# Performance work log

Hardware: AMD Instinct MI355X
Metric: run time of the kernel (lower is better)

The kernel has to match this reference:

```python
import jax, jax.numpy as jnp
import numpy as np

NEG_SLOPE = 0.2
LN_EPS = 1e-5


def setup_inputs() -> dict:
    key = jax.random.key(0)
    k1, k2, k3, k4 = jax.random.split(key, 4)
    B, K, D, H = 64, 256, 1024, 2
    x = jax.random.normal(k1, (B, K, D), dtype=jnp.float32)
    adj = jax.random.randint(k2, (K, K), 0, 2, dtype=jnp.int32)
    # Xavier-ish scaling for weights
    W = jax.random.normal(k3, (D, D), dtype=jnp.float32) * (1.0 / np.sqrt(D))
    a = jax.random.normal(k4, (H, 2 * D), dtype=jnp.float32) * (1.0 / np.sqrt(2 * D))
    gamma = jnp.ones((D,), dtype=jnp.float32)
    beta = jnp.zeros((D,), dtype=jnp.float32)
    return {"x": x, "adj": adj, "W": W, "a": a, "gamma": gamma, "beta": beta}


def _layer_norm(y, gamma, beta):
    mu = jnp.mean(y, axis=-1, keepdims=True)
    var = jnp.mean(jnp.square(y - mu), axis=-1, keepdims=True)
    return (y - mu) * jax.lax.rsqrt(var + LN_EPS) * gamma + beta


def reference(x, adj, W, a, gamma, beta):
    # x: (B,K,D), adj: (K,K), W: (D,D), a: (H,2D)
    D = W.shape[1]
    h = jnp.einsum("bki,io->bko", x, W)  # (B,K,D)
    # GAT trick: a^T [h_i; h_j] = a_src . h_i + a_dst . h_j (same math as
    # the huge pairwise-concat + Linear in the original module).
    a_src, a_dst = a[:, :D], a[:, D:]  # each (H,D)
    f_i = jnp.einsum("bkd,hd->bhk", h, a_src)  # (B,H,K)
    f_j = jnp.einsum("bkd,hd->bhk", h, a_dst)  # (B,H,K)
    e = f_i[:, :, :, None] + f_j[:, :, None, :]  # (B,H,K,K)
    e = jnp.where(e >= 0, e, NEG_SLOPE * e)  # LeakyReLU
    mask = (adj != 0)[None, None]  # (1,1,K,K)
    e = jnp.where(mask, e, -jnp.inf)
    attn = jax.nn.softmax(e, axis=-1)
    attn = jnp.where(jnp.isnan(attn), 0.0, attn)  # nan_to_num for all-masked rows
    # dropout is identity in eval mode
    head_out = jnp.einsum("bhij,bjd->bhid", attn, h)  # (B,H,K,D)
    out = jnp.mean(head_out, axis=1)  # average heads, (B,K,D)
    out = _layer_norm(out + x, gamma, beta)  # residual is Identity (in_dim==out_dim)
    return out
```

## Files before the change

### kernel.cpp

```cpp
#include <hip/hip_runtime.h>
#include <hip/hip_bf16.h>

#define KN 256
#define DD 1024
#define HH 2

typedef __attribute__((ext_vector_type(8))) short short8;
typedef __attribute__((ext_vector_type(4))) float f32x4;

__device__ __forceinline__ ushort f2b(float f) {
  union { float f; unsigned u; } v; v.f = f;
  unsigned u = v.u;
  return (ushort)((u + 0x7fffu + ((u >> 16) & 1u)) >> 16);
}
__device__ __forceinline__ float b2f(ushort h) {
  union { unsigned u; float f; } v; v.u = ((unsigned)h) << 16;
  return v.f;
}
__device__ __forceinline__ void gload16(const ushort* g, ushort* l) {
  __builtin_amdgcn_global_load_lds(
      (const __attribute__((address_space(1))) void*)g,
      (__attribute__((address_space(3))) void*)l, 16, 0, 0);
}

__global__ __launch_bounds__(256) void k_conv(const float* __restrict__ x,
                                              ushort* __restrict__ xb) {
  int c0 = blockIdx.x * 256 + threadIdx.x;
  for (int it = 0; it < 4; ++it) {
    size_t i = ((size_t)c0 + (size_t)it * 524288) * 8;
    float4 v0 = *reinterpret_cast<const float4*>(&x[i]);
    float4 v1 = *reinterpret_cast<const float4*>(&x[i + 4]);
    short8 o;
    o[0] = (short)f2b(v0.x); o[1] = (short)f2b(v0.y);
    o[2] = (short)f2b(v0.z); o[3] = (short)f2b(v0.w);
    o[4] = (short)f2b(v1.x); o[5] = (short)f2b(v1.y);
    o[6] = (short)f2b(v1.z); o[7] = (short)f2b(v1.w);
    *reinterpret_cast<short8*>(&xb[i]) = o;
  }
}

__global__ __launch_bounds__(256) void k_wT(const float* __restrict__ W, ushort* __restrict__ WTb) {
  __shared__ float t[32][33];
  int tx = threadIdx.x, ty = threadIdx.y;
  int x = blockIdx.x * 32 + tx;
  int y0 = blockIdx.y * 32 + ty;
  for (int i = 0; i < 32; i += 8)
    t[ty + i][tx] = W[(size_t)(y0 + i) * DD + x];
  __syncthreads();
  int xo = blockIdx.y * 32 + tx;
  int yo = blockIdx.x * 32 + ty;
  for (int i = 0; i < 32; i += 8)
    WTb[(size_t)(yo + i) * DD + xo] = f2b(t[tx][ty + i]);
}

__device__ __forceinline__ void gh_stage(const ushort* gA0, const ushort* gB0, int kt,
                                         ushort* As, ushort* Bs, int tid) {
  int wb = tid & ~63;
  for (int it = 0; it < 2; ++it) {
    int slot = it * 256 + tid;
    int row = slot >> 2, kc = slot & 3;
    int kcs = kc ^ (((row >> 1) & 1) << 1);
    gload16(gA0 + (size_t)row * DD + kt + kcs * 8, As + (size_t)(it * 256 + wb) * 8);
    gload16(gB0 + (size_t)row * DD + kt + kcs * 8, Bs + (size_t)(it * 256 + wb) * 8);
  }
}

__global__ __launch_bounds__(256) void k_gemm_h(const ushort* __restrict__ xb,
                                                const ushort* __restrict__ WTb,
                                                ushort* __restrict__ hT) {
  __shared__ ushort As[2][4096];
  __shared__ ushort Bs[2][4096];
  const int tid = threadIdx.x;
  const int bm = blockIdx.x;
  const int bn = blockIdx.y;
  const int w = tid >> 6, lane = tid & 63;
  const int wm = (w >> 1) * 64, wn = (w & 1) * 64;
  const int r16 = lane & 15, kqi = lane >> 4;
  const ushort* gA0 = xb + (size_t)(bm * 128) * DD;
  const ushort* gB0 = WTb + (size_t)(bn * 128) * DD;
  f32x4 acc[4][4] = {};

  gh_stage(gA0, gB0, 0, As[0], Bs[0], tid);
  __syncthreads();
  for (int kt = 0; kt < DD; kt += 32) {
    int cur = (kt >> 5) & 1;
    if (kt + 32 < DD)
      gh_stage(gA0, gB0, kt + 32, As[cur ^ 1], Bs[cur ^ 1], tid);
    const ushort* Ac = As[cur];
    const ushort* Bc = Bs[cur];
    short8 af[4], bf[4];
    for (int mf = 0; mf < 4; ++mf) {
      int row = wm + mf * 16 + r16;
      af[mf] = *reinterpret_cast<const short8*>(Ac + row * 32 + (kqi ^ (((row >> 1) & 1) << 1)) * 8);
    }
    for (int nf = 0; nf < 4; ++nf) {
      int row = wn + nf * 16 + r16;
      bf[nf] = *reinterpret_cast<const short8*>(Bc + row * 32 + (kqi ^ (((row >> 1) & 1) << 1)) * 8);
    }
    for (int mf = 0; mf < 4; ++mf)
      for (int nf = 0; nf < 4; ++nf)
        acc[mf][nf] = __builtin_amdgcn_mfma_f32_16x16x32_bf16(af[mf], bf[nf], acc[mf][nf], 0, 0, 0);
    __syncthreads();
  }
  const int b = bm >> 1;
  const int j0base = (bm & 1) * 128 + wm;
  for (int mf = 0; mf < 4; ++mf) {
    int j0 = j0base + mf * 16 + (lane >> 4) * 4;
    for (int nf = 0; nf < 4; ++nf) {
      int C = bn * 128 + wn + nf * 16 + r16;
      ushort4 o;
      o.x = f2b(acc[mf][nf][0]); o.y = f2b(acc[mf][nf][1]);
      o.z = f2b(acc[mf][nf][2]); o.w = f2b(acc[mf][nf][3]);
      *reinterpret_cast<ushort4*>(&hT[((size_t)b * DD + C) * KN + j0]) = o;
    }
  }
}

__global__ __launch_bounds__(256) void k_f(const ushort* __restrict__ hT,
                                           const float* __restrict__ a,
                                           float* __restrict__ fip, float* __restrict__ fjp) {
  __shared__ float als[4][256];
  int b = blockIdx.x, dq = blockIdx.y;
  int tid = threadIdx.x;
  for (int v = 0; v < 4; ++v) als[v][tid] = a[v * DD + dq * 256 + tid];
  __syncthreads();
  const ushort* base = hT + ((size_t)b * DD + dq * 256) * KN + tid;
  float a0 = 0.f, a1 = 0.f, a2 = 0.f, a3 = 0.f;
  #pragma unroll 8
  for (int d = 0; d < 256; ++d) {
    float hv = b2f(base[(size_t)d * KN]);
    a0 += hv * als[0][d];
    a1 += hv * als[1][d];
    a2 += hv * als[2][d];
    a3 += hv * als[3][d];
  }
  size_t o = ((size_t)(dq * 64 + b) * HH) * KN + tid;
  fip[o] = a0;
  fjp[o] = a1;
  fip[o + KN] = a2;
  fjp[o + KN] = a3;
}

__global__ __launch_bounds__(256) void k_attn(const float* __restrict__ fip, const float* __restrict__ fjp,
                                              const int* __restrict__ adj, ushort* __restrict__ Pb) {
  int w = threadIdx.x >> 6, l = threadIdx.x & 63;
  int gw = blockIdx.x * 4 + w;
  int b = gw >> 8, i = gw & 255;
  int4 am = *reinterpret_cast<const int4*>(adj + i * KN + l * 4);
  int msk[4] = { am.x, am.y, am.z, am.w };
  float fi0 = 0.f, fi1 = 0.f;
  float fj0[4] = {0.f, 0.f, 0.f, 0.f}, fj1[4] = {0.f, 0.f, 0.f, 0.f};
  for (int dq = 0; dq < 4; ++dq) {
    size_t o = ((size_t)(dq * 64 + b) * HH) * KN;
    fi0 += fip[o + i];
    fi1 += fip[o + KN + i];
    float4 t0 = *reinterpret_cast<const float4*>(&fjp[o + l * 4]);
    float4 t1 = *reinterpret_cast<const float4*>(&fjp[o + KN + l * 4]);
    fj0[0] += t0.x; fj0[1] += t0.y; fj0[2] += t0.z; fj0[3] += t0.w;
    fj1[0] += t1.x; fj1[1] += t1.y; fj1[2] += t1.z; fj1[3] += t1.w;
  }
  float e0[4], e1[4];
  const float NEGINF = -3.0e38f;
  float m0 = NEGINF, m1 = NEGINF;
  for (int e = 0; e < 4; ++e) {
    float v0 = fi0 + fj0[e], v1 = fi1 + fj1[e];
    v0 = v0 >= 0.f ? v0 : 0.2f * v0;
    v1 = v1 >= 0.f ? v1 : 0.2f * v1;
    e0[e] = v0; e1[e] = v1;
    if (msk[e]) { m0 = fmaxf(m0, v0); m1 = fmaxf(m1, v1); }
  }
  for (int off = 1; off < 64; off <<= 1) {
    m0 = fmaxf(m0, __shfl_xor(m0, off));
    m1 = fmaxf(m1, __shfl_xor(m1, off));
  }
  float p0[4], p1[4], s0 = 0.f, s1 = 0.f;
  for (int e = 0; e < 4; ++e) {
    p0[e] = msk[e] ? __expf(e0[e] - m0) : 0.f;
    p1[e] = msk[e] ? __expf(e1[e] - m1) : 0.f;
    s0 += p0[e]; s1 += p1[e];
  }
  for (int off = 1; off < 64; off <<= 1) {
    s0 += __shfl_xor(s0, off);
    s1 += __shfl_xor(s1, off);
  }
  float i0 = s0 > 0.f ? 1.f / s0 : 0.f;
  float i1 = s1 > 0.f ? 1.f / s1 : 0.f;
  ushort4 o;
  o.x = f2b(0.5f * (p0[0] * i0 + p1[0] * i1));
  o.y = f2b(0.5f * (p0[1] * i0 + p1[1] * i1));
  o.z = f2b(0.5f * (p0[2] * i0 + p1[2] * i1));
  o.w = f2b(0.5f * (p0[3] * i0 + p1[3] * i1));
  *reinterpret_cast<ushort4*>(&Pb[((size_t)b * KN + i) * KN + l * 4]) = o;
}

__global__ __launch_bounds__(512) void k_gemm_o(const ushort* __restrict__ Pb,
                                                const ushort* __restrict__ hT,
                                                const float* __restrict__ x,
                                                ushort* __restrict__ y,
                                                float* __restrict__ pstats) {
  __shared__ ushort As[2][8192];
  __shared__ ushort Bs[2][4096];
  __shared__ float red2[256][2][2];
  const int b = blockIdx.x;
  const int dt = blockIdx.y;
  const int tid = threadIdx.x;
  const int w = tid >> 6, lane = tid & 63;
  const int wm = (w >> 1) * 64;
  const int wn = (w & 1) * 64;
  const int r16 = lane & 15, kqi = lane >> 4;
  const ushort* PbB = Pb + (size_t)b * KN * KN;
  const ushort* hTB = hT + ((size_t)b * DD + dt * 128) * KN;
  f32x4 acc[4][4] = {};

  const int wb = tid & ~63;
  #define OSTAGE(buf, kt)                                                          \
    {                                                                              \
      for (int it = 0; it < 2; ++it) {                                             \
        int slot = it * 512 + tid;                                                 \
        int row = slot >> 2, kc = slot & 3;                                        \
        int kcs = kc ^ (((row >> 1) & 1) << 1);                                    \
        gload16(PbB + (size_t)row * KN + (kt) + kcs * 8,                           \
                As[buf] + (size_t)(it * 512 + wb) * 8);                            \
      }                                                                            \
      {                                                                            \
        int row = tid >> 2, kc = tid & 3;                                          \
        int kcs = kc ^ (((row >> 1) & 1) << 1);                                    \
        gload16(hTB + (size_t)row * KN + (kt) + kcs * 8,                           \
                Bs[buf] + (size_t)wb * 8);                                         \
      }                                                                            \
    }

  OSTAGE(0, 0);
  __syncthreads();
  for (int kt = 0; kt < KN; kt += 32) {
    int cur = (kt >> 5) & 1;
    if (kt + 32 < KN)
      OSTAGE(cur ^ 1, kt + 32);
    const ushort* Ac = As[cur];
    const ushort* Bc = Bs[cur];
    short8 af[4], bf[4];
    for (int mf = 0; mf < 4; ++mf) {
      int row = wm + mf * 16 + r16;
      af[mf] = *reinterpret_cast<const short8*>(Ac + (size_t)row * 32 + (kqi ^ (((row >> 1) & 1) << 1)) * 8);
    }
    for (int nf = 0; nf < 4; ++nf) {
      int row = wn + nf * 16 + r16;
      bf[nf] = *reinterpret_cast<const short8*>(Bc + (size_t)row * 32 + (kqi ^ (((row >> 1) & 1) << 1)) * 8);
    }
    for (int mf = 0; mf < 4; ++mf)
      for (int nf = 0; nf < 4; ++nf)
        acc[mf][nf] = __builtin_amdgcn_mfma_f32_16x16x32_bf16(af[mf], bf[nf], acc[mf][nf], 0, 0, 0);
    __syncthreads();
  }
  #undef OSTAGE

  const int g = lane >> 4;
  float ps[4][4] = {}, qs[4][4] = {};
  #pragma unroll
  for (int mf = 0; mf < 4; ++mf)
    #pragma unroll
    for (int nf = 0; nf < 4; ++nf) {
      int C = dt * 128 + wn + nf * 16 + r16;
      #pragma unroll
      for (int rr = 0; rr < 4; ++rr) {
        int i = wm + mf * 16 + g * 4 + rr;
        size_t gi = ((size_t)(b * KN + i)) * DD + C;
        float v = acc[mf][nf][rr] + x[gi];
        y[gi] = f2b(v);
        ps[mf][rr] += v; qs[mf][rr] += v * v;
      }
    }
  #pragma unroll
  for (int off = 1; off < 16; off <<= 1)
    #pragma unroll
    for (int mf = 0; mf < 4; ++mf)
      #pragma unroll
      for (int rr = 0; rr < 4; ++rr) {
        ps[mf][rr] += __shfl_xor(ps[mf][rr], off);
        qs[mf][rr] += __shfl_xor(qs[mf][rr], off);
      }
  if (r16 == 0) {
    #pragma unroll
    for (int mf = 0; mf < 4; ++mf)
      #pragma unroll
      for (int rr = 0; rr < 4; ++rr) {
        int i = wm + mf * 16 + g * 4 + rr;
        red2[i][w & 1][0] = ps[mf][rr];
        red2[i][w & 1][1] = qs[mf][rr];
      }
  }
  __syncthreads();
  if (tid < 256) {
    float S = red2[tid][0][0] + red2[tid][1][0];
    float Q = red2[tid][0][1] + red2[tid][1][1];
    size_t o = ((size_t)(dt * 64 + b) * KN + tid) * 2;
    pstats[o] = S;
    pstats[o + 1] = Q;
  }
}

__global__ __launch_bounds__(256) void k_ln(const ushort* __restrict__ y,
                                            const float* __restrict__ pstats,
                                            const float* __restrict__ gamma,
                                            const float* __restrict__ beta,
                                            float* __restrict__ out) {
  int tid = threadIdx.x;
  size_t row = blockIdx.x;
  int b = (int)(row >> 8), i = (int)(row & 255);
  float S = 0.f, Q = 0.f;
  #pragma unroll
  for (int dt = 0; dt < 8; ++dt) {
    size_t o = ((size_t)(dt * 64 + b) * KN + i) * 2;
    S += pstats[o];
    Q += pstats[o + 1];
  }
  float mu = S * (1.0f / DD);
  float var = Q * (1.0f / DD) - mu * mu;
  float inv = rsqrtf(var + 1e-5f);
  ushort4 v = *reinterpret_cast<const ushort4*>(&y[row * DD + tid * 4]);
  float4 gm = *reinterpret_cast<const float4*>(&gamma[tid * 4]);
  float4 bt = *reinterpret_cast<const float4*>(&beta[tid * 4]);
  float4 o;
  o.x = (b2f(v.x) - mu) * inv * gm.x + bt.x;
  o.y = (b2f(v.y) - mu) * inv * gm.y + bt.y;
  o.z = (b2f(v.z) - mu) * inv * gm.z + bt.z;
  o.w = (b2f(v.w) - mu) * inv * gm.w + bt.w;
  *reinterpret_cast<float4*>(&out[row * DD + tid * 4]) = o;
}

extern "C" void kernel_launch(void* const* d_in, const int* in_sizes, int n_in,
                              void* d_out, int out_size, void* d_ws, size_t ws_size,
                              hipStream_t stream) {
  const float* x     = (const float*)d_in[0];
  const int*   adj   = (const int*)d_in[1];
  const float* W     = (const float*)d_in[2];
  const float* a     = (const float*)d_in[3];
  const float* gamma = (const float*)d_in[4];
  const float* beta  = (const float*)d_in[5];
  float* out = (float*)d_out;

  char* ws = (char*)d_ws;
  const size_t OFS_WT = 0;
  const size_t OFS_XB = 2097152;
  const size_t OFS_HT = 35651584;
  const size_t OFS_PB = 69206016;
  const size_t NEED   = 77856768;
  if (ws_size < NEED) return;

  ushort* WTb   = (ushort*)(ws + OFS_WT);
  float*  fip   = (float*)(ws + OFS_WT);
  float*  fjp   = (float*)(ws + OFS_WT + 524288);
  float*  pst   = (float*)(ws + OFS_WT);
  ushort* xb    = (ushort*)(ws + OFS_XB);
  ushort* y     = (ushort*)(ws + OFS_XB);
  ushort* hT    = (ushort*)(ws + OFS_HT);
  ushort* Pb    = (ushort*)(ws + OFS_PB);

  k_conv<<<2048, 256, 0, stream>>>(x, xb);
  k_wT<<<dim3(32, 32), dim3(32, 8), 0, stream>>>(W, WTb);
  k_gemm_h<<<dim3(128, 8), 256, 0, stream>>>(xb, WTb, hT);
  k_f<<<dim3(64, 4), 256, 0, stream>>>(hT, a, fip, fjp);
  k_attn<<<4096, 256, 0, stream>>>(fip, fjp, adj, Pb);
  k_gemm_o<<<dim3(64, 8), 512, 0, stream>>>(Pb, hT, x, y, pst);
  k_ln<<<16384, 256, 0, stream>>>(y, pst, gamma, beta, out);
}
```

Before: 143.8 us.

## Deepen GEMM prefetch with manual waitcnt barriers and read bf16 residual

Both MFMA GEMM kernels now issue two stages of async global-to-LDS loads up front. Each iteration waits with an explicit s_waitcnt vmcnt before a raw s_barrier, so the next stage's loads stay in flight during compute. The LDS XOR swizzle is removed, which simplifies addressing but may bring back bank conflicts. When the workspace is large enough, the output GEMM reads the residual from the bf16 copy of x instead of fp32 and writes y to a separate region, halving residual traffic at some precision cost.

```diff
diff --git a/kernel.cpp b/kernel.cpp
--- a/kernel.cpp
+++ b/kernel.cpp
@@ -56,12 +56,12 @@
 __device__ __forceinline__ void gh_stage(const ushort* gA0, const ushort* gB0, int kt,
                                          ushort* As, ushort* Bs, int tid) {
   int wb = tid & ~63;
+  #pragma unroll
   for (int it = 0; it < 2; ++it) {
     int slot = it * 256 + tid;
     int row = slot >> 2, kc = slot & 3;
-    int kcs = kc ^ (((row >> 1) & 1) << 1);
-    gload16(gA0 + (size_t)row * DD + kt + kcs * 8, As + (size_t)(it * 256 + wb) * 8);
-    gload16(gB0 + (size_t)row * DD + kt + kcs * 8, Bs + (size_t)(it * 256 + wb) * 8);
+    gload16(gA0 + (size_t)row * DD + kt + kc * 8, As + (size_t)(it * 256 + wb) * 8);
+    gload16(gB0 + (size_t)row * DD + kt + kc * 8, Bs + (size_t)(it * 256 + wb) * 8);
   }
 }
 
@@ -81,31 +81,42 @@
   f32x4 acc[4][4] = {};
 
   gh_stage(gA0, gB0, 0, As[0], Bs[0], tid);
-  __syncthreads();
-  for (int kt = 0; kt < DD; kt += 32) {
-    int cur = (kt >> 5) & 1;
-    if (kt + 32 < DD)
-      gh_stage(gA0, gB0, kt + 32, As[cur ^ 1], Bs[cur ^ 1], tid);
+  gh_stage(gA0, gB0, 32, As[1], Bs[1], tid);
+  for (int it = 0; it < 32; ++it) {
+    const int cur = it & 1;
+    if (it < 31) asm volatile("s_waitcnt vmcnt(4)" ::: "memory");
+    else         asm volatile("s_waitcnt vmcnt(0)" ::: "memory");
+    __builtin_amdgcn_s_barrier();
+    __builtin_amdgcn_sched_barrier(0);
     const ushort* Ac = As[cur];
     const ushort* Bc = Bs[cur];
     short8 af[4], bf[4];
+    #pragma unroll
     for (int mf = 0; mf < 4; ++mf) {
       int row = wm + mf * 16 + r16;
-      af[mf] = *reinterpret_cast<const short8*>(Ac + row * 32 + (kqi ^ (((row >> 1) & 1) << 1)) * 8);
-    }
+      af[mf] = *reinterpret_cast<const short8*>(Ac + (size_t)row * 32 + kqi * 8);
+    }
+    #pragma unroll
     for (int nf = 0; nf < 4; ++nf) {
       int row = wn + nf * 16 + r16;
-      bf[nf] = *reinterpret_cast<const short8*>(Bc + row * 32 + (kqi ^ (((row >> 1) & 1) << 1)) * 8);
-    }
+      bf[nf] = *reinterpret_cast<const short8*>(Bc + (size_t)row * 32 + kqi * 8);
+    }
+    #pragma unroll
     for (int mf = 0; mf < 4; ++mf)
+      #pragma unroll
       for (int nf = 0; nf < 4; ++nf)
         acc[mf][nf] = __builtin_amdgcn_mfma_f32_16x16x32_bf16(af[mf], bf[nf], acc[mf][nf], 0, 0, 0);
-    __syncthreads();
+    __builtin_amdgcn_sched_barrier(0);
+    __builtin_amdgcn_s_barrier();
+    if (it < 30)
+      gh_stage(gA0, gB0, (it + 2) * 32, As[cur], Bs[cur], tid);
   }
   const int b = bm >> 1;
   const int j0base = (bm & 1) * 128 + wm;
+  #pragma unroll
   for (int mf = 0; mf < 4; ++mf) {
     int j0 = j0base + mf * 16 + (lane >> 4) * 4;
+    #pragma unroll
     for (int nf = 0; nf < 4; ++nf) {
       int C = bn * 128 + wn + nf * 16 + r16;
       ushort4 o;
@@ -196,6 +207,8 @@
 __global__ __launch_bounds__(512) void k_gemm_o(const ushort* __restrict__ Pb,
                                                 const ushort* __restrict__ hT,
                                                 const float* __restrict__ x,
+                                                const ushort* __restrict__ xb,
+                                                int use_xb,
                                                 ushort* __restrict__ y,
                                                 float* __restrict__ pstats) {
   __shared__ ushort As[2][8192];
@@ -211,46 +224,54 @@
   const ushort* PbB = Pb + (size_t)b * KN * KN;
   const ushort* hTB = hT + ((size_t)b * DD + dt * 128) * KN;
   f32x4 acc[4][4] = {};
-
   const int wb = tid & ~63;
+
   #define OSTAGE(buf, kt)                                                          \
     {                                                                              \
-      for (int it = 0; it < 2; ++it) {                                             \
-        int slot = it * 512 + tid;                                                 \
+      _Pragma("unroll")                                                            \
+      for (int s = 0; s < 2; ++s) {                                                \
+        int slot = s * 512 + tid;                                                  \
         int row = slot >> 2, kc = slot & 3;                                        \
-        int kcs = kc ^ (((row >> 1) & 1) << 1);                                    \
-        gload16(PbB + (size_t)row * KN + (kt) + kcs * 8,                           \
-                As[buf] + (size_t)(it * 512 + wb) * 8);                            \
+        gload16(PbB + (size_t)row * KN + (kt) + kc * 8,                            \
+                As[buf] + (size_t)(s * 512 + wb) * 8);                             \
       }                                                                            \
       {                                                                            \
         int row = tid >> 2, kc = tid & 3;                                          \
-        int kcs = kc ^ (((row >> 1) & 1) << 1);                                    \
-        gload16(hTB + (size_t)row * KN + (kt) + kcs * 8,                           \
+        gload16(hTB + (size_t)row * KN + (kt) + kc * 8,                            \
                 Bs[buf] + (size_t)wb * 8);                                         \
       }                                                                            \
     }
 
   OSTAGE(0, 0);
-  __syncthreads();
-  for (int kt = 0; kt < KN; kt += 32) {
-    int cur = (kt >> 5) & 1;
-    if (kt + 32 < KN)
-      OSTAGE(cur ^ 1, kt + 32);
+  OSTAGE(1, 32);
+  for (int it8 = 0; it8 < 8; ++it8) {
+    const int cur = it8 & 1;
+    if (it8 < 7) asm volatile("s_waitcnt vmcnt(3)" ::: "memory");
+    else         asm volatile("s_waitcnt vmcnt(0)" ::: "memory");
+    __builtin_amdgcn_s_barrier();
+    __builtin_amdgcn_sched_barrier(0);
     const ushort* Ac = As[cur];
     const ushort* Bc = Bs[cur];
     short8 af[4], bf[4];
+    #pragma unroll
     for (int mf = 0; mf < 4; ++mf) {
       int row = wm + mf * 16 + r16;
-      af[mf] = *reinterpret_cast<const short8*>(Ac + (size_t)row * 32 + (kqi ^ (((row >> 1) & 1) << 1)) * 8);
-    }
+      af[mf] = *reinterpret_cast<const short8*>(Ac + (size_t)row * 32 + kqi * 8);
+    }
+    #pragma unroll
     for (int nf = 0; nf < 4; ++nf) {
       int row = wn + nf * 16 + r16;
-      bf[nf] = *reinterpret_cast<const short8*>(Bc + (size_t)row * 32 + (kqi ^ (((row >> 1) & 1) << 1)) * 8);
-    }
+      bf[nf] = *reinterpret_cast<const short8*>(Bc + (size_t)row * 32 + kqi * 8);
+    }
+    #pragma unroll
     for (int mf = 0; mf < 4; ++mf)
+      #pragma unroll
       for (int nf = 0; nf < 4; ++nf)
         acc[mf][nf] = __builtin_amdgcn_mfma_f32_16x16x32_bf16(af[mf], bf[nf], acc[mf][nf], 0, 0, 0);
-    __syncthreads();
+    __builtin_amdgcn_sched_barrier(0);
+    __builtin_amdgcn_s_barrier();
+    if (it8 < 6)
+      OSTAGE(cur, (it8 + 2) * 32);
   }
   #undef OSTAGE
 
@@ -265,7 +286,8 @@
       for (int rr = 0; rr < 4; ++rr) {
         int i = wm + mf * 16 + g * 4 + rr;
         size_t gi = ((size_t)(b * KN + i)) * DD + C;
-        float v = acc[mf][nf][rr] + x[gi];
+        float rv = use_xb ? b2f(xb[gi]) : x[gi];
+        float v = acc[mf][nf][rr] + rv;
         y[gi] = f2b(v);
         ps[mf][rr] += v; qs[mf][rr] += v * v;
       }
@@ -344,23 +366,25 @@
   const size_t OFS_XB = 2097152;
   const size_t OFS_HT = 35651584;
   const size_t OFS_PB = 69206016;
-  const size_t NEED   = 77856768;
+  const size_t NEED     = 77856768;
+  const size_t NEED_BIG = 111411200;
   if (ws_size < NEED) return;
+  const int use_xb = (ws_size >= NEED_BIG) ? 1 : 0;
 
   ushort* WTb   = (ushort*)(ws + OFS_WT);
   float*  fip   = (float*)(ws + OFS_WT);
   float*  fjp   = (float*)(ws + OFS_WT + 524288);
   float*  pst   = (float*)(ws + OFS_WT);
   ushort* xb    = (ushort*)(ws + OFS_XB);
-  ushort* y     = (ushort*)(ws + OFS_XB);
   ushort* hT    = (ushort*)(ws + OFS_HT);
   ushort* Pb    = (ushort*)(ws + OFS_PB);
+  ushort* y     = use_xb ? (ushort*)(ws + NEED) : (ushort*)(ws + OFS_XB);
 
   k_conv<<<2048, 256, 0, stream>>>(x, xb);
   k_wT<<<dim3(32, 32), dim3(32, 8), 0, stream>>>(W, WTb);
   k_gemm_h<<<dim3(128, 8), 256, 0, stream>>>(xb, WTb, hT);
   k_f<<<dim3(64, 4), 256, 0, stream>>>(hT, a, fip, fjp);
   k_attn<<<4096, 256, 0, stream>>>(fip, fjp, adj, Pb);
-  k_gemm_o<<<dim3(64, 8), 512, 0, stream>>>(Pb, hT, x, y, pst);
+  k_gemm_o<<<dim3(64, 8), 512, 0, stream>>>(Pb, hT, x, xb, use_xb, y, pst);
   k_ln<<<16384, 256, 0, stream>>>(y, pst, gamma, beta, out);
 }
```

After: 140.6 us. 2.2% less time.
